# Kernel tuning notes

Hardware: AMD Instinct MI355X
Metric: run time of the kernel (lower is better)

The kernel has to match this reference:

```python
import jax, jax.numpy as jnp
import numpy as np

NUM_TAGS = 9
INNER_DIM = 64
HIDDEN = 768
MASK_VAL = 1e12


def setup_inputs() -> dict:
    key = jax.random.key(0)
    k1, k2, k3, k4 = jax.random.split(key, 4)
    B, S = 16, 512
    encoder_output = jax.random.normal(k1, (B, S, HIDDEN), dtype=jnp.float32)
    token_ids = jax.random.randint(k2, (B, S), 0, 30000, dtype=jnp.int64)
    attention_mask = jnp.ones((B, S), dtype=jnp.int32)
    W = jax.random.normal(k3, (HIDDEN, NUM_TAGS * INNER_DIM * 2), dtype=jnp.float32) * 0.02
    b = jax.random.normal(k4, (NUM_TAGS * INNER_DIM * 2,), dtype=jnp.float32) * 0.02
    return {"encoder_output": encoder_output, "token_ids": token_ids,
            "attention_mask": attention_mask, "W": W, "b": b}


def _rope_sin_cos(seq_len, dim, dtype):
    # sinusoidal position embedding, interleaved then repeat_interleave(2)
    pos = jnp.arange(seq_len, dtype=dtype)[:, None]              # [S,1]
    inv = jnp.power(10000.0, -2.0 * jnp.arange(dim // 2, dtype=dtype) / dim)
    ang = pos * inv                                              # [S,d/2]
    sin = jnp.repeat(jnp.sin(ang), 2, axis=-1)                   # [S,d]
    cos = jnp.repeat(jnp.cos(ang), 2, axis=-1)                   # [S,d]
    return sin, cos


def _rotate_half(x):
    # stack([-x[...,1::2], x[...,::2]], -1).reshape(x.shape)
    x2 = jnp.stack([-x[..., 1::2], x[..., ::2]], axis=-1)
    return x2.reshape(x.shape)


def reference(encoder_output, token_ids, attention_mask, W, b):
    B, S, _ = encoder_output.shape
    d = INNER_DIM
    out = encoder_output @ W + b                                 # [B,S,T*2d]
    out = out.reshape(B, S, NUM_TAGS, 2 * d)
    qw, kw = out[..., :d], out[..., d:]                          # [B,S,T,d]

    sin, cos = _rope_sin_cos(S, d, encoder_output.dtype)
    sin = sin[None, :, None, :]                                  # [1,S,1,d]
    cos = cos[None, :, None, :]
    qw = qw * cos + _rotate_half(qw) * sin
    kw = kw * cos + _rotate_half(kw) * sin

    logits = jnp.einsum('bshd,bthd->bhst', qw, kw)               # [B,T,S,S]

    pad = attention_mask.astype(logits.dtype)[:, None, None, :]  # key-side mask
    logits = logits * pad - (1.0 - pad) * MASK_VAL
    tril = jnp.tril(jnp.ones((S, S), dtype=logits.dtype), -1)
    logits = logits - tril * MASK_VAL
    return logits / jnp.sqrt(jnp.asarray(d, logits.dtype))
```

## Files before the change

### kernel.cpp

```cpp
#include <hip/hip_runtime.h>

#define MASK_VALF 1000000000000.0f

typedef __attribute__((ext_vector_type(8))) short s16x8;
typedef __attribute__((ext_vector_type(4))) float f32x4;

__device__ __forceinline__ short f2bf(float f) {
    union { float f; unsigned u; } v; v.f = f;
    unsigned r = (v.u + 0x7FFFu + ((v.u >> 16) & 1u)) >> 16;
    return (short)(r & 0xFFFFu);
}

#define GLOAD16(gp, lp) __builtin_amdgcn_global_load_lds( \
    (const __attribute__((address_space(1))) void*)(gp),  \
    (__attribute__((address_space(3))) void*)(lp), 16, 0, 0)

__global__ void prep_enc(const float* __restrict__ enc, short* __restrict__ encb, int n4) {
    int i = blockIdx.x * blockDim.x + threadIdx.x;
    if (i < n4) {
        float4 v = ((const float4*)enc)[i];
        short4 o;
        o.x = f2bf(v.x); o.y = f2bf(v.y); o.z = f2bf(v.z); o.w = f2bf(v.w);
        ((short4*)encb)[i] = o;
    }
}

__global__ void transpose_w(const float* __restrict__ W, short* __restrict__ Wt) {
    __shared__ float tile[32][33];
    int n = blockIdx.x * 32 + threadIdx.x;
    int k = blockIdx.y * 32 + threadIdx.y;
    tile[threadIdx.y][threadIdx.x] = W[k * 1152 + n];
    __syncthreads();
    int n2 = blockIdx.x * 32 + threadIdx.y;
    int k2 = blockIdx.y * 32 + threadIdx.x;
    Wt[n2 * 768 + k2] = f2bf(tile[threadIdx.x][threadIdx.y]);
}

__global__ void sincos_tab(float2* __restrict__ sc) {
    int id = blockIdx.x * blockDim.x + threadIdx.x;
    int pos = id >> 5, j = id & 31;
    float inv = powf(10000.0f, -2.0f * (float)j / 64.0f);
    float ang = (float)pos * inv;
    float s, c;
    sincosf(ang, &s, &c);
    sc[id] = make_float2(c, s);
}

__global__ __launch_bounds__(256) void gemm1_rope(
    const short* __restrict__ A,
    const short* __restrict__ Bt,
    const float* __restrict__ bias,
    const float2* __restrict__ sc,
    short* __restrict__ qk)
{
    __shared__ __align__(16) short As[128 * 32];
    __shared__ __align__(16) short Bs[128 * 32];
    const int t = threadIdx.x;
    const int w = t >> 6, lane = t & 63;
    const int lr = lane & 15, quad = lane >> 4;
    const int wm = w >> 1, wn = w & 1;
    const int m0 = blockIdx.y * 128;
    const int n0 = blockIdx.x * 128;

    f32x4 acc[4][4] = {};

    const short* gA = A  + (size_t)(m0 + (t >> 2)) * 768 + (t & 3) * 8;
    const short* gB = Bt + (size_t)(n0 + (t >> 2)) * 768 + (t & 3) * 8;
    short* lA0 = &As[w * 512];
    short* lA1 = &As[2048 + w * 512];
    short* lB0 = &Bs[w * 512];
    short* lB1 = &Bs[2048 + w * 512];

    for (int kt = 0; kt < 24; ++kt) {
        __syncthreads();
        GLOAD16(gA,            lA0);
        GLOAD16(gA + 64 * 768, lA1);
        GLOAD16(gB,            lB0);
        GLOAD16(gB + 64 * 768, lB1);
        gA += 32; gB += 32;
        __syncthreads();

        s16x8 af[4], bw[4];
#pragma unroll
        for (int i = 0; i < 4; ++i)
            af[i] = *(const s16x8*)&As[(wm * 64 + i * 16 + lr) * 32 + quad * 8];
#pragma unroll
        for (int j = 0; j < 4; ++j)
            bw[j] = *(const s16x8*)&Bs[(wn * 64 + j * 16 + lr) * 32 + quad * 8];
#pragma unroll
        for (int i = 0; i < 4; ++i)
#pragma unroll
            for (int j = 0; j < 4; ++j)
                acc[i][j] = __builtin_amdgcn_mfma_f32_16x16x32_bf16(af[i], bw[j], acc[i][j], 0, 0, 0);
    }

#pragma unroll
    for (int j = 0; j < 4; ++j) {
        const int colg = n0 + wn * 64 + j * 16 + lr;
        const float bv = bias[colg];
        const int tag = colg >> 7;
        const int qkf = (colg >> 6) & 1;
        const int dd  = colg & 63;
        const int jj  = dd >> 1;
        const int odd = colg & 1;
#pragma unroll
        for (int i = 0; i < 4; ++i) {
#pragma unroll
            for (int r = 0; r < 4; ++r) {
                const int rowg = m0 + wm * 64 + i * 16 + quad * 4 + r;
                const int bidx = rowg >> 9;
                const int pos  = rowg & 511;
                float v = acc[i][j][r] + bv;
                float p = __shfl_xor(v, 1, 64);
                float2 cs = sc[pos * 32 + jj];
                float o = odd ? fmaf(v, cs.x, p * cs.y)
                              : fmaf(v, cs.x, -p * cs.y);
                qk[((((size_t)bidx * 9 + tag) * 2 + qkf) * 512 + pos) * 64 + dd] = f2bf(o);
            }
        }
    }
}

__global__ __launch_bounds__(256) void gemm2_mask(
    const short* __restrict__ qk,
    const int* __restrict__ amask,
    float* __restrict__ out)
{
    __shared__ __align__(16) short Qs[128 * 64];
    __shared__ __align__(16) short Ks[128 * 64];
    const int t = threadIdx.x;
    const int w = t >> 6, lane = t & 63;
    const int lr = lane & 15, quad = lane >> 4;
    const int wm = w >> 1, wn = w & 1;
    const int bh = blockIdx.z;
    const int bidx = bh / 9;
    const int s0 = blockIdx.y * 128;
    const int t0 = blockIdx.x * 128;

    const short* qbase = qk + (size_t)bh * 2 * 512 * 64;
    const short* kbase = qbase + 512 * 64;

    const int row = t >> 3, col8 = (t & 7) * 8;
#pragma unroll
    for (int p = 0; p < 4; ++p) {
        GLOAD16(qbase + (size_t)(s0 + p * 32 + row) * 64 + col8, &Qs[p * 2048 + w * 512]);
        GLOAD16(kbase + (size_t)(t0 + p * 32 + row) * 64 + col8, &Ks[p * 2048 + w * 512]);
    }
    __syncthreads();

    f32x4 acc[4][4] = {};
#pragma unroll
    for (int kk = 0; kk < 64; kk += 32) {
        s16x8 af[4], bw[4];
#pragma unroll
        for (int i = 0; i < 4; ++i)
            af[i] = *(const s16x8*)&Qs[(wm * 64 + i * 16 + lr) * 64 + kk + quad * 8];
#pragma unroll
        for (int j = 0; j < 4; ++j)
            bw[j] = *(const s16x8*)&Ks[(wn * 64 + j * 16 + lr) * 64 + kk + quad * 8];
#pragma unroll
        for (int i = 0; i < 4; ++i)
#pragma unroll
            for (int j = 0; j < 4; ++j)
                acc[i][j] = __builtin_amdgcn_mfma_f32_16x16x32_bf16(af[i], bw[j], acc[i][j], 0, 0, 0);
    }

#pragma unroll
    for (int j = 0; j < 4; ++j) {
        const int tg = t0 + wn * 64 + j * 16 + lr;
        const float padf = (float)amask[bidx * 512 + tg];
        const float mk = (1.0f - padf) * MASK_VALF;
#pragma unroll
        for (int i = 0; i < 4; ++i) {
#pragma unroll
            for (int r = 0; r < 4; ++r) {
                const int sg = s0 + wm * 64 + i * 16 + quad * 4 + r;
                float v = acc[i][j][r] * padf - mk - (sg > tg ? MASK_VALF : 0.0f);
                out[((size_t)bh * 512 + sg) * 512 + tg] = v * 0.125f;
            }
        }
    }
}

extern "C" void kernel_launch(void* const* d_in, const int* in_sizes, int n_in,
                              void* d_out, int out_size, void* d_ws, size_t ws_size,
                              hipStream_t stream) {
    const float* enc   = (const float*)d_in[0];
    const int*   amask = (const int*)d_in[2];
    const float* W     = (const float*)d_in[3];
    const float* bias  = (const float*)d_in[4];
    float* out = (float*)d_out;

    char* ws = (char*)d_ws;
    short*  encb = (short*)(ws);
    short*  wtb  = (short*)(ws + 12582912);
    float2* sc   = (float2*)(ws + 14352384);
    short*  qk   = (short*)(ws + 14483456);

    prep_enc  <<<6144, 256, 0, stream>>>(enc, encb, 1572864);
    transpose_w<<<dim3(36, 24), dim3(32, 32), 0, stream>>>(W, wtb);
    sincos_tab<<<64, 256, 0, stream>>>(sc);
    gemm1_rope<<<dim3(9, 64), 256, 0, stream>>>(encb, wtb, bias, sc, qk);
    gemm2_mask<<<dim3(4, 4, 144), 256, 0, stream>>>(qk, amask, out);
}
```

Baseline: 235.4 us.

## Merge prep kernels and swap MFMA operands for vectorized epilogue stores

The three prep kernels (bf16 cast, W transpose, sincos table) become one launch dispatched by block index. In both GEMMs the A and B operands are swapped so each lane's four accumulator values lie along contiguous output columns. This lets the epilogues use float4 bias/sincos/mask loads, packed int2 bf16 stores for q/k, and float4 stores for the large fp32 logits output. It removes two launches and many scalar uncoalesced stores, at the cost of a more intricate index mapping.

```diff
diff --git a/kernel.cpp b/kernel.cpp
--- a/kernel.cpp
+++ b/kernel.cpp
@@ -5,52 +5,63 @@
 typedef __attribute__((ext_vector_type(8))) short s16x8;
 typedef __attribute__((ext_vector_type(4))) float f32x4;
 
-__device__ __forceinline__ short f2bf(float f) {
+__device__ __forceinline__ unsigned f2bf_u(float f) {
     union { float f; unsigned u; } v; v.f = f;
-    unsigned r = (v.u + 0x7FFFu + ((v.u >> 16) & 1u)) >> 16;
-    return (short)(r & 0xFFFFu);
-}
+    return (v.u + 0x7FFFu + ((v.u >> 16) & 1u)) >> 16;
+}
+__device__ __forceinline__ short f2bf(float f) { return (short)(f2bf_u(f) & 0xFFFFu); }
 
 #define GLOAD16(gp, lp) __builtin_amdgcn_global_load_lds( \
     (const __attribute__((address_space(1))) void*)(gp),  \
     (__attribute__((address_space(3))) void*)(lp), 16, 0, 0)
 
-__global__ void prep_enc(const float* __restrict__ enc, short* __restrict__ encb, int n4) {
-    int i = blockIdx.x * blockDim.x + threadIdx.x;
-    if (i < n4) {
+__global__ __launch_bounds__(256) void prep_all(
+    const float* __restrict__ enc, short* __restrict__ encb,
+    const float* __restrict__ W, short* __restrict__ wtb,
+    float* __restrict__ scf)
+{
+    const int blk = blockIdx.x;
+    const int t = threadIdx.x;
+    if (blk < 6144) {
+        int i = blk * 256 + t;
         float4 v = ((const float4*)enc)[i];
         short4 o;
         o.x = f2bf(v.x); o.y = f2bf(v.y); o.z = f2bf(v.z); o.w = f2bf(v.w);
         ((short4*)encb)[i] = o;
-    }
-}
-
-__global__ void transpose_w(const float* __restrict__ W, short* __restrict__ Wt) {
-    __shared__ float tile[32][33];
-    int n = blockIdx.x * 32 + threadIdx.x;
-    int k = blockIdx.y * 32 + threadIdx.y;
-    tile[threadIdx.y][threadIdx.x] = W[k * 1152 + n];
-    __syncthreads();
-    int n2 = blockIdx.x * 32 + threadIdx.y;
-    int k2 = blockIdx.y * 32 + threadIdx.x;
-    Wt[n2 * 768 + k2] = f2bf(tile[threadIdx.x][threadIdx.y]);
-}
-
-__global__ void sincos_tab(float2* __restrict__ sc) {
-    int id = blockIdx.x * blockDim.x + threadIdx.x;
-    int pos = id >> 5, j = id & 31;
-    float inv = powf(10000.0f, -2.0f * (float)j / 64.0f);
-    float ang = (float)pos * inv;
-    float s, c;
-    sincosf(ang, &s, &c);
-    sc[id] = make_float2(c, s);
+    } else if (blk < 7008) {
+        __shared__ float tile[32][33];
+        int tb = blk - 6144;
+        int tbx = tb % 36;
+        int tby = tb / 36;
+        int tx = t & 31, ty = t >> 5;
+#pragma unroll
+        for (int r = 0; r < 4; ++r) {
+            int row = ty + r * 8;
+            tile[row][tx] = W[(tby * 32 + row) * 1152 + tbx * 32 + tx];
+        }
+        __syncthreads();
+#pragma unroll
+        for (int r = 0; r < 4; ++r) {
+            int row = ty + r * 8;
+            wtb[(size_t)(tbx * 32 + row) * 768 + tby * 32 + tx] = f2bf(tile[tx][row]);
+        }
+    } else {
+        int id = (blk - 7008) * 256 + t;
+        int pos = id >> 5, j = id & 31;
+        float inv = powf(10000.0f, -2.0f * (float)j / 64.0f);
+        float ang = (float)pos * inv;
+        float s, c;
+        sincosf(ang, &s, &c);
+        scf[id * 2]     = c;
+        scf[id * 2 + 1] = s;
+    }
 }
 
 __global__ __launch_bounds__(256) void gemm1_rope(
     const short* __restrict__ A,
     const short* __restrict__ Bt,
     const float* __restrict__ bias,
-    const float2* __restrict__ sc,
+    const float* __restrict__ scf,
     short* __restrict__ qk)
 {
     __shared__ __align__(16) short As[128 * 32];
@@ -83,10 +94,10 @@
         s16x8 af[4], bw[4];
 #pragma unroll
         for (int i = 0; i < 4; ++i)
-            af[i] = *(const s16x8*)&As[(wm * 64 + i * 16 + lr) * 32 + quad * 8];
+            af[i] = *(const s16x8*)&Bs[(wm * 64 + i * 16 + lr) * 32 + quad * 8];
 #pragma unroll
         for (int j = 0; j < 4; ++j)
-            bw[j] = *(const s16x8*)&Bs[(wn * 64 + j * 16 + lr) * 32 + quad * 8];
+            bw[j] = *(const s16x8*)&As[(wn * 64 + j * 16 + lr) * 32 + quad * 8];
 #pragma unroll
         for (int i = 0; i < 4; ++i)
 #pragma unroll
@@ -95,28 +106,32 @@
     }
 
 #pragma unroll
-    for (int j = 0; j < 4; ++j) {
-        const int colg = n0 + wn * 64 + j * 16 + lr;
-        const float bv = bias[colg];
-        const int tag = colg >> 7;
-        const int qkf = (colg >> 6) & 1;
-        const int dd  = colg & 63;
-        const int jj  = dd >> 1;
-        const int odd = colg & 1;
-#pragma unroll
-        for (int i = 0; i < 4; ++i) {
-#pragma unroll
-            for (int r = 0; r < 4; ++r) {
-                const int rowg = m0 + wm * 64 + i * 16 + quad * 4 + r;
-                const int bidx = rowg >> 9;
-                const int pos  = rowg & 511;
-                float v = acc[i][j][r] + bv;
-                float p = __shfl_xor(v, 1, 64);
-                float2 cs = sc[pos * 32 + jj];
-                float o = odd ? fmaf(v, cs.x, p * cs.y)
-                              : fmaf(v, cs.x, -p * cs.y);
-                qk[((((size_t)bidx * 9 + tag) * 2 + qkf) * 512 + pos) * 64 + dd] = f2bf(o);
-            }
+    for (int i = 0; i < 4; ++i) {
+        const int colg0 = n0 + wm * 64 + i * 16 + quad * 4;
+        const float4 bv = *(const float4*)&bias[colg0];
+        const int tag = colg0 >> 7;
+        const int qkf = (colg0 >> 6) & 1;
+        const int dd0 = colg0 & 63;
+        const int jj0 = dd0 >> 1;
+        short* qbase = qk + ((size_t)tag * 2 + qkf) * 512 * 64 + dd0;
+#pragma unroll
+        for (int j = 0; j < 4; ++j) {
+            const int rowg = m0 + wn * 64 + j * 16 + lr;
+            const int bidx = rowg >> 9;
+            const int pos  = rowg & 511;
+            const float4 cs = *(const float4*)&scf[pos * 64 + jj0 * 2];
+            float x0 = acc[i][j][0] + bv.x;
+            float x1 = acc[i][j][1] + bv.y;
+            float x2 = acc[i][j][2] + bv.z;
+            float x3 = acc[i][j][3] + bv.w;
+            float o0 = x0 * cs.x - x1 * cs.y;
+            float o1 = x1 * cs.x + x0 * cs.y;
+            float o2 = x2 * cs.z - x3 * cs.w;
+            float o3 = x3 * cs.z + x2 * cs.w;
+            int2 st;
+            st.x = (int)(f2bf_u(o0) & 0xFFFFu) | (int)(f2bf_u(o1) << 16);
+            st.y = (int)(f2bf_u(o2) & 0xFFFFu) | (int)(f2bf_u(o3) << 16);
+            *(int2*)&qbase[((size_t)bidx * 9 * 2 * 512 + pos) * 64] = st;
         }
     }
 }
@@ -154,10 +169,10 @@
         s16x8 af[4], bw[4];
 #pragma unroll
         for (int i = 0; i < 4; ++i)
-            af[i] = *(const s16x8*)&Qs[(wm * 64 + i * 16 + lr) * 64 + kk + quad * 8];
+            af[i] = *(const s16x8*)&Ks[(wm * 64 + i * 16 + lr) * 64 + kk + quad * 8];
 #pragma unroll
         for (int j = 0; j < 4; ++j)
-            bw[j] = *(const s16x8*)&Ks[(wn * 64 + j * 16 + lr) * 64 + kk + quad * 8];
+            bw[j] = *(const s16x8*)&Qs[(wn * 64 + j * 16 + lr) * 64 + kk + quad * 8];
 #pragma unroll
         for (int i = 0; i < 4; ++i)
 #pragma unroll
@@ -166,18 +181,21 @@
     }
 
 #pragma unroll
-    for (int j = 0; j < 4; ++j) {
-        const int tg = t0 + wn * 64 + j * 16 + lr;
-        const float padf = (float)amask[bidx * 512 + tg];
-        const float mk = (1.0f - padf) * MASK_VALF;
-#pragma unroll
-        for (int i = 0; i < 4; ++i) {
-#pragma unroll
-            for (int r = 0; r < 4; ++r) {
-                const int sg = s0 + wm * 64 + i * 16 + quad * 4 + r;
-                float v = acc[i][j][r] * padf - mk - (sg > tg ? MASK_VALF : 0.0f);
-                out[((size_t)bh * 512 + sg) * 512 + tg] = v * 0.125f;
-            }
+    for (int i = 0; i < 4; ++i) {
+        const int tg0 = t0 + wm * 64 + i * 16 + quad * 4;
+        const int4 am = *(const int4*)&amask[bidx * 512 + tg0];
+        const float4 pad = make_float4((float)am.x, (float)am.y, (float)am.z, (float)am.w);
+        const float4 mk = make_float4((1.0f - pad.x) * MASK_VALF, (1.0f - pad.y) * MASK_VALF,
+                                      (1.0f - pad.z) * MASK_VALF, (1.0f - pad.w) * MASK_VALF);
+#pragma unroll
+        for (int j = 0; j < 4; ++j) {
+            const int sg = s0 + wn * 64 + j * 16 + lr;
+            float4 v;
+            v.x = (acc[i][j][0] * pad.x - mk.x - (sg > tg0     ? MASK_VALF : 0.0f)) * 0.125f;
+            v.y = (acc[i][j][1] * pad.y - mk.y - (sg > tg0 + 1 ? MASK_VALF : 0.0f)) * 0.125f;
+            v.z = (acc[i][j][2] * pad.z - mk.z - (sg > tg0 + 2 ? MASK_VALF : 0.0f)) * 0.125f;
+            v.w = (acc[i][j][3] * pad.w - mk.w - (sg > tg0 + 3 ? MASK_VALF : 0.0f)) * 0.125f;
+            *(float4*)&out[((size_t)bh * 512 + sg) * 512 + tg0] = v;
         }
     }
 }
@@ -192,14 +210,12 @@
     float* out = (float*)d_out;
 
     char* ws = (char*)d_ws;
-    short*  encb = (short*)(ws);
-    short*  wtb  = (short*)(ws + 12582912);
-    float2* sc   = (float2*)(ws + 14352384);
-    short*  qk   = (short*)(ws + 14483456);
-
-    prep_enc  <<<6144, 256, 0, stream>>>(enc, encb, 1572864);
-    transpose_w<<<dim3(36, 24), dim3(32, 32), 0, stream>>>(W, wtb);
-    sincos_tab<<<64, 256, 0, stream>>>(sc);
-    gemm1_rope<<<dim3(9, 64), 256, 0, stream>>>(encb, wtb, bias, sc, qk);
+    short* encb = (short*)(ws);
+    short* wtb  = (short*)(ws + 12582912);
+    float* scf  = (float*)(ws + 14352384);
+    short* qk   = (short*)(ws + 14483456);
+
+    prep_all  <<<7072, 256, 0, stream>>>(enc, encb, W, wtb, scf);
+    gemm1_rope<<<dim3(9, 64), 256, 0, stream>>>(encb, wtb, bias, scf, qk);
     gemm2_mask<<<dim3(4, 4, 144), 256, 0, stream>>>(qk, amask, out);
 }
```

After: 225.9 us. 4.0% less time.
